# Optimization experiments

Hardware: AMD Instinct MI355X
Metric: run time of the kernel (lower is better)

Reference implementation:

```python
import jax, jax.numpy as jnp
import numpy as np
import itertools


def exclude_mask(n, d):
    # Boolean mask over d object axes of size n: True iff all indices pairwise distinct.
    if d <= 1:
        return jnp.ones((n,) * d, dtype=bool)
    idx = [jnp.arange(n).reshape((1,) * i + (n,) + (1,) * (d - 1 - i)) for i in range(d)]
    m = jnp.ones((n,) * d, dtype=bool)
    for i in range(d):
        for j in range(i + 1, d):
            m = m & (idx[i] != idx[j])
    return m


def reduce_group(x, d, exclude_self=True):
    # x: [B, n^d (d object axes), C] -> [B, n^(d-1), 2C]
    # exists = max over last object axis (masked to 0), forall = min (masked to 1),
    # interleaved per channel as in torch.stack(..., dim=-1).view(..., 2C).
    if exclude_self and d > 1:
        n = x.shape[1]
        m = exclude_mask(n, d)[None, ..., None]
        x0 = jnp.where(m, x, 0.0)
        x1 = jnp.where(m, x, 1.0)
    else:
        x0 = x1 = x
    ex = jnp.max(x0, axis=-2)
    fa = jnp.min(x1, axis=-2)
    out = jnp.stack([ex, fa], axis=-1)  # [..., C, 2]
    return out.reshape(out.shape[:-2] + (out.shape[-2] * 2,))


def expand_group(x, n):
    # Insert a new object axis of size n just before the channel axis (broadcast).
    return jnp.broadcast_to(jnp.expand_dims(x, -2), x.shape[:-1] + (n, x.shape[-1]))


def permute_group(x, d):
    # Concatenate all d! permutations of the last d object axes along channels.
    if d <= 1:
        return x
    nd = x.ndim
    obj_axes = list(range(nd - 1 - d, nd - 1))
    res = []
    for perm in itertools.permutations(obj_axes):
        p = list(range(0, nd - 1 - d)) + list(perm) + [nd - 1]
        res.append(jnp.transpose(x, p))
    return jnp.concatenate(res, axis=-1)


def mlp(x, W1, b1, W2, b2):
    # InferenceLayer: Linear -> ReLU -> Linear -> Sigmoid, applied on channel dim.
    h = jax.nn.relu(x @ W1 + b1)
    return jax.nn.sigmoid(h @ W2 + b2)


def setup_inputs() -> dict:
    key = jax.random.key(0)
    ks = jax.random.split(key, 24)
    B, n, C, H = 4, 48, 16, 64
    cin = {0: 48, 1: 64, 2: 128, 3: 192}
    inp = {
        "x0": jax.random.uniform(ks[0], (B, C), dtype=jnp.float32),
        "x1": jax.random.uniform(ks[1], (B, n, C), dtype=jnp.float32),
        "x2": jax.random.uniform(ks[2], (B, n, n, C), dtype=jnp.float32),
        "x3": jax.random.uniform(ks[3], (B, n, n, n, C), dtype=jnp.float32),
    }
    for g in range(4):
        inp[f"W1_{g}"] = 0.05 * jax.random.normal(ks[4 + 4 * g], (cin[g], H), dtype=jnp.float32)
        inp[f"b1_{g}"] = jnp.zeros((H,), dtype=jnp.float32)
        inp[f"W2_{g}"] = 0.05 * jax.random.normal(ks[5 + 4 * g], (H, C), dtype=jnp.float32)
        inp[f"b2_{g}"] = jnp.zeros((C,), dtype=jnp.float32)
    return inp


def reference(x0, x1, x2, x3,
              W1_0, b1_0, W2_0, b2_0,
              W1_1, b1_1, W2_1, b2_1,
              W1_2, b1_2, W2_2, b2_2,
              W1_3, b1_3, W2_3, b2_3):
    n = x1.shape[1]
    # group 0: [self, reduce(group1)] -> MLP
    t0 = jnp.concatenate([x0, reduce_group(x1, 1)], axis=-1)            # [B, 48]
    o0 = mlp(t0, W1_0, b1_0, W2_0, b2_0)
    # group 1: [expand(group0), self, reduce(group2)] -> MLP (permuter d=1 is identity)
    t1 = jnp.concatenate([expand_group(x0, n), x1, reduce_group(x2, 2)], axis=-1)  # [B,n,64]
    o1 = mlp(t1, W1_1, b1_1, W2_1, b2_1)
    # group 2: [expand(group1), self, reduce(group3)] -> permute(d=2) -> MLP
    t2 = jnp.concatenate([expand_group(x1, n), x2, reduce_group(x3, 3)], axis=-1)  # [B,n,n,64]
    t2 = permute_group(t2, 2)                                           # [B,n,n,128]
    o2 = mlp(t2, W1_2, b1_2, W2_2, b2_2)
    # group 3: [expand(group2), self] -> permute(d=3) -> MLP
    t3 = jnp.concatenate([expand_group(x2, n), x3], axis=-1)            # [B,n,n,n,32]
    t3 = permute_group(t3, 3)                                           # [B,n,n,n,192]
    o3 = mlp(t3, W1_3, b1_3, W2_3, b2_3)
    return (o0, o1, o2, o3)
```

## Files before the change

kernel.cpp:

```cpp
#include <hip/hip_runtime.h>
#include <math.h>

#define NN 48

typedef __attribute__((ext_vector_type(8))) short bf16x8;
typedef __attribute__((ext_vector_type(4))) float f32x4;

__device__ __forceinline__ float sigmoidf_(float x) {
    return 1.0f / (1.0f + __expf(-x));
}

__device__ __forceinline__ unsigned short f2bf(float f) {
    unsigned u = __float_as_uint(f);
    return (unsigned short)((u + 0x7fffu + ((u >> 16) & 1u)) >> 16);
}

__device__ __forceinline__ unsigned packbf2(float a, float b) {
    return (unsigned)f2bf(a) | ((unsigned)f2bf(b) << 16);
}

__global__ __launch_bounds__(256) void k_pre(const float* __restrict__ x3,
                                             const float* __restrict__ W1, const float* __restrict__ W2,
                                             float* __restrict__ r3, unsigned short* __restrict__ wf) {
    int tid = threadIdx.x;
    if (blockIdx.x == 0) {
        for (int e = tid; e < 13312; e += 256) {
            unsigned short v;
            if (e < 12288) {
                int idx = e & 7, l = (e >> 3) & 63, r = e >> 9;
                int ks = r % 6, nt = r / 6;
                v = f2bf(W1[(ks * 32 + ((l >> 4) << 3) + idx) * 64 + (nt << 4) + (l & 15)]);
            } else {
                int e2 = e - 12288;
                int idx = e2 & 7, l = (e2 >> 3) & 63, ks = e2 >> 9;
                v = f2bf(W2[(ks * 32 + ((l >> 4) << 3) + idx) * 16 + (l & 15)]);
            }
            wf[e] = v;
        }
        return;
    }
    int idx = (blockIdx.x - 1) * 256 + tid;
    int cq = idx & 3;
    int pos = idx >> 2;
    int j = pos % NN;
    int i = (pos / NN) % NN;
    const float* base = x3 + (size_t)pos * NN * 16 + (cq << 2);
    float4 ex = make_float4(0.f, 0.f, 0.f, 0.f);
    float4 fa = make_float4(1.f, 1.f, 1.f, 1.f);
    bool dead = (i == j);
    #pragma unroll 8
    for (int k = 0; k < NN; ++k) {
        float4 v = *(const float4*)(base + k * 16);
        bool ok = !dead && (k != i) && (k != j);
        ex.x = fmaxf(ex.x, ok ? v.x : 0.f);  fa.x = fminf(fa.x, ok ? v.x : 1.f);
        ex.y = fmaxf(ex.y, ok ? v.y : 0.f);  fa.y = fminf(fa.y, ok ? v.y : 1.f);
        ex.z = fmaxf(ex.z, ok ? v.z : 0.f);  fa.z = fminf(fa.z, ok ? v.z : 1.f);
        ex.w = fmaxf(ex.w, ok ? v.w : 0.f);  fa.w = fminf(fa.w, ok ? v.w : 1.f);
    }
    float* dst = r3 + (size_t)pos * 32 + (cq << 3);
    *(float4*)dst       = make_float4(ex.x, fa.x, ex.y, fa.y);
    *(float4*)(dst + 4) = make_float4(ex.z, fa.z, ex.w, fa.w);
}

__global__ __launch_bounds__(256) void k_conv(const float* __restrict__ x2, const float* __restrict__ x3,
                                              unsigned short* __restrict__ x2bf,
                                              unsigned short* __restrict__ x3bf) {
    int e = blockIdx.x * 256 + threadIdx.x;
    int stride = gridDim.x * 256;
    for (; e < 1806336; e += stride) {
        const float* src;
        unsigned short* dst;
        if (e < 36864) { int off = e << 2;           src = x2 + off; dst = x2bf + off; }
        else           { int off = (e - 36864) << 2; src = x3 + off; dst = x3bf + off; }
        float4 v = *(const float4*)src;
        uint2 pk;
        pk.x = packbf2(v.x, v.y);
        pk.y = packbf2(v.z, v.w);
        *(uint2*)dst = pk;
    }
}

__global__ __launch_bounds__(256) void k_small(const float* __restrict__ x0, const float* __restrict__ x1,
        const float* __restrict__ x2, const float* __restrict__ r3,
        const float* __restrict__ W1_0, const float* __restrict__ b1_0,
        const float* __restrict__ W2_0, const float* __restrict__ b2_0,
        const float* __restrict__ W1_1, const float* __restrict__ b1_1,
        const float* __restrict__ W2_1, const float* __restrict__ b2_1,
        const float* __restrict__ W1_2, const float* __restrict__ b1_2,
        const float* __restrict__ W2_2, const float* __restrict__ b2_2,
        float* __restrict__ out) {
    __shared__ __align__(16) float smem[8960];
    int tid = threadIdx.x;
    int blk = blockIdx.x;
    if (blk == 0) {
        float* st0 = smem;
        float* sh0 = smem + 192;
        int b = tid >> 6, sub = (tid >> 4) & 3, c = tid & 15;
        float ex = -INFINITY, fa = INFINITY;
        for (int ii = sub * 12; ii < sub * 12 + 12; ++ii) {
            float v = x1[(b * NN + ii) * 16 + c];
            ex = fmaxf(ex, v); fa = fminf(fa, v);
        }
        ex = fmaxf(ex, __shfl_xor(ex, 16)); fa = fminf(fa, __shfl_xor(fa, 16));
        ex = fmaxf(ex, __shfl_xor(ex, 32)); fa = fminf(fa, __shfl_xor(fa, 32));
        if (sub == 0) { st0[b * 48 + 16 + 2 * c] = ex; st0[b * 48 + 17 + 2 * c] = fa; }
        if (tid < 64) st0[(tid >> 4) * 48 + (tid & 15)] = x0[tid];
        __syncthreads();
        {
            int bb = tid >> 6, ln = tid & 63;
            float h = b1_0[ln];
            for (int cc = 0; cc < 48; ++cc) h += st0[bb * 48 + cc] * W1_0[cc * 64 + ln];
            sh0[bb * 64 + ln] = fmaxf(h, 0.f);
        }
        __syncthreads();
        if (tid < 64) {
            int bb = tid >> 4, o = tid & 15;
            float acc = b2_0[o];
            for (int tt = 0; tt < 64; ++tt) acc += sh0[bb * 64 + tt] * W2_0[tt * 16 + o];
            out[bb * 16 + o] = sigmoidf_(acc);
        }
    } else if (blk <= 48) {
        int grp = tid >> 6, ln = tid & 63;
        int row = (blk - 1) * 4 + grp;
        int b = row / NN, i = row % NN;
        float* sin1 = smem + grp * 64;
        float* sh1  = smem + 256 + grp * 64;
        int c = ln & 15, q = ln >> 4;
        float ex = 0.f, fa = 1.f;
        const float* xb = x2 + (size_t)row * NN * 16 + c;
        for (int jj = q * 12; jj < q * 12 + 12; ++jj) {
            float v = xb[jj * 16];
            bool ok = (jj != i);
            ex = fmaxf(ex, ok ? v : 0.f); fa = fminf(fa, ok ? v : 1.f);
        }
        ex = fmaxf(ex, __shfl_xor(ex, 16)); fa = fminf(fa, __shfl_xor(fa, 16));
        ex = fmaxf(ex, __shfl_xor(ex, 32)); fa = fminf(fa, __shfl_xor(fa, 32));
        if (q == 0) { sin1[32 + 2 * c] = ex; sin1[33 + 2 * c] = fa; }
        if (ln < 16) sin1[ln] = x0[b * 16 + ln];
        else if (ln < 32) sin1[ln] = x1[row * 16 + (ln - 16)];
        __syncthreads();
        float h = b1_1[ln];
        #pragma unroll
        for (int c4 = 0; c4 < 64; c4 += 4) {
            float4 iv = *(const float4*)&sin1[c4];
            h += iv.x * W1_1[(c4 + 0) * 64 + ln] + iv.y * W1_1[(c4 + 1) * 64 + ln]
               + iv.z * W1_1[(c4 + 2) * 64 + ln] + iv.w * W1_1[(c4 + 3) * 64 + ln];
        }
        sh1[ln] = fmaxf(h, 0.f);
        __syncthreads();
        if (ln < 16) {
            float acc = b2_1[ln];
            #pragma unroll
            for (int tt = 0; tt < 64; ++tt) acc += sh1[tt] * W2_1[tt * 16 + ln];
            out[64 + row * 16 + ln] = sigmoidf_(acc);
        }
    } else {
        float* sW1  = smem;
        float* sin_ = smem + 8192;
        float* sh   = smem + 8704;
        int wv = tid >> 6, ln = tid & 63;
        for (int p = tid; p < 8192; p += 256) sW1[p] = W1_2[p];
        float bias = b1_2[ln];
        __syncthreads();
        for (int rr = 0; rr < 4; ++rr) {
            int row = (blk - 49) * 16 + rr * 4 + wv;
            int j = row % NN;
            int bi = row / NN;
            int i = bi % NN;
            int b = bi / NN;
            for (int cc = ln; cc < 128; cc += 64) {
                int half = cc >> 6, w = cc & 63;
                int a1 = half ? j : i;
                int a2 = half ? i : j;
                float v;
                if (w < 16)      v = x1[(b * NN + a1) * 16 + w];
                else if (w < 32) v = x2[((b * NN + a1) * NN + a2) * 16 + (w - 16)];
                else             v = r3[((size_t)(b * NN + a1) * NN + a2) * 32 + (w - 32)];
                sin_[wv * 128 + cc] = v;
            }
            __syncthreads();
            float h = bias;
            #pragma unroll
            for (int c4 = 0; c4 < 128; c4 += 4) {
                float4 iv = *(const float4*)&sin_[wv * 128 + c4];
                h += iv.x * sW1[(c4 + 0) * 64 + ln] + iv.y * sW1[(c4 + 1) * 64 + ln]
                   + iv.z * sW1[(c4 + 2) * 64 + ln] + iv.w * sW1[(c4 + 3) * 64 + ln];
            }
            sh[wv * 64 + ln] = fmaxf(h, 0.f);
            __syncthreads();
            if (ln < 16) {
                float acc = b2_2[ln];
                #pragma unroll
                for (int tt = 0; tt < 64; ++tt) acc += sh[wv * 64 + tt] * W2_2[tt * 16 + ln];
                out[3136 + row * 16 + ln] = sigmoidf_(acc);
            }
            __syncthreads();
        }
    }
}

__global__ __launch_bounds__(256) void k_g3d(const unsigned short* __restrict__ x2bf,
        const unsigned short* __restrict__ x3bf, const unsigned short* __restrict__ wf,
        const float* __restrict__ b1, const float* __restrict__ b2,
        float* __restrict__ out3) {
    __shared__ __align__(16) unsigned short sH[2][6 * 64 * 8];

    int tid = threadIdx.x, wv = tid >> 6, l = tid & 63;
    int pp = blockIdx.x, i = 0;
    while (pp >= NN - i) { pp -= NN - i; ++i; }
    int j = i + pp;
    int b = blockIdx.y;

    bf16x8 w1f[6];
    #pragma unroll
    for (int ks = 0; ks < 6; ++ks)
        w1f[ks] = *(const bf16x8*)(wf + (((wv * 6 + ks) << 6) + l) * 8);
    bf16x8 w2f[2];
    #pragma unroll
    for (int ks = 0; ks < 2; ++ks)
        w2f[ks] = *(const bf16x8*)(wf + 12288 + ((ks << 6) + l) * 8);

    const int b2b = b * 36864;
    const int b3b = b * 1769472;
    const int cb2_[6] = { b2b + (i * NN + j) * 16, b2b + i * 768, b2b + (j * NN + i) * 16,
                          b2b + i * 16,            b2b + j * 768, b2b + j * 16 };
    const int cb3_[6] = { b3b + (i * NN + j) * 768, b3b + i * 36864 + j * 16, b3b + (j * NN + i) * 768,
                          b3b + i * 768 + j * 16,   b3b + j * 36864 + i * 16, b3b + j * 768 + i * 16 };
    const int s2_[6] = { 0, 16, 0, 768, 16, 768 };
    const int s3_[6] = { 16, 768, 16, 36864, 768, 36864 };

    int l15 = l & 15, g = l >> 4;
    bool isx2 = (g < 2);
    int goff = (g & 1) << 3;
    const unsigned short* bp = isx2 ? x2bf : x3bf;
    int off_[6], st_[6];
    #pragma unroll
    for (int f = 0; f < 6; ++f) {
        int s = isx2 ? s2_[f] : s3_[f];
        int base = isx2 ? cb2_[f] : cb3_[f];
        off_[f] = base + l15 * s + goff;
        st_[f] = s << 4;
    }

    float bv = b1[(wv << 4) + l15];
    f32x4 acc0_0 = {bv, bv, bv, bv};
    f32x4 acc0_1 = acc0_0, acc0_2 = acc0_0;
    f32x4 acc1_0 = acc0_0, acc1_1 = acc0_0, acc1_2 = acc0_0;
    const int p1[6] = { 2, 4, 0, 5, 1, 3 };

    #pragma unroll
    for (int mt = 0; mt < 3; ++mt) {
        f32x4 a0 = (mt == 0) ? acc0_0 : (mt == 1) ? acc0_1 : acc0_2;
        f32x4 a1 = (mt == 0) ? acc1_0 : (mt == 1) ? acc1_1 : acc1_2;
        #pragma unroll
        for (int f = 0; f < 6; ++f) {
            bf16x8 a = *(const bf16x8*)(bp + off_[f] + mt * st_[f]);
            a0 = __builtin_amdgcn_mfma_f32_16x16x32_bf16(a, w1f[f], a0, 0, 0, 0);
            a1 = __builtin_amdgcn_mfma_f32_16x16x32_bf16(a, w1f[p1[f]], a1, 0, 0, 0);
        }
        if (mt == 0) { acc0_0 = a0; acc1_0 = a1; }
        else if (mt == 1) { acc0_1 = a0; acc1_1 = a1; }
        else { acc0_2 = a0; acc1_2 = a1; }
    }

    {
        int within = ((wv & 1) << 4) + l15;
        int ks2 = wv >> 1;
        int lhi = (within >> 3) << 4;
        int idx = within & 7;
        int rbase = (l >> 4) << 2;
        #pragma unroll
        for (int tr = 0; tr < 2; ++tr) {
            #pragma unroll
            for (int mt = 0; mt < 3; ++mt) {
                f32x4 a = tr ? ((mt == 0) ? acc1_0 : (mt == 1) ? acc1_1 : acc1_2)
                             : ((mt == 0) ? acc0_0 : (mt == 1) ? acc0_1 : acc0_2);
                #pragma unroll
                for (int rg = 0; rg < 4; ++rg) {
                    float h = fmaxf(a[rg], 0.0f);
                    int lp = rbase + rg + lhi;
                    sH[tr][((((mt << 1) + ks2) << 6) + lp) * 8 + idx] = f2bf(h);
                }
            }
        }
    }
    __syncthreads();

    if (wv < 3) {
        float bv2 = b2[l15];
        #pragma unroll
        for (int tr = 0; tr < 2; ++tr) {
            if (tr == 0 || i != j) {
                f32x4 acc = {bv2, bv2, bv2, bv2};
                #pragma unroll
                for (int ks = 0; ks < 2; ++ks) {
                    bf16x8 a = *(const bf16x8*)&sH[tr][((((wv << 1) + ks) << 6) + l) << 3];
                    acc = __builtin_amdgcn_mfma_f32_16x16x32_bf16(a, w2f[ks], acc, 0, 0, 0);
                }
                int triple = tr ? ((b * NN + j) * NN + i) : ((b * NN + i) * NN + j);
                size_t obase = ((size_t)triple * NN + (wv << 4) + ((l >> 4) << 2)) * 16 + l15;
                #pragma unroll
                for (int rg = 0; rg < 4; ++rg)
                    out3[obase + (size_t)rg * 16] = sigmoidf_(acc[rg]);
            }
        }
    }
}

__global__ __launch_bounds__(256) void k_g3m(const float* __restrict__ x2, const float* __restrict__ x3,
                                             const unsigned short* __restrict__ wf,
                                             const float* __restrict__ b1, const float* __restrict__ b2,
                                             float* __restrict__ out3) {
    __shared__ __align__(16) unsigned short sA[18 * 64 * 8];
    __shared__ __align__(16) unsigned short sH[6 * 64 * 8];

    int tid = threadIdx.x;
    int wv = tid >> 6, l = tid & 63;
    int triple = blockIdx.x;
    int j = triple % NN;
    int bi = triple / NN;
    int i = bi % NN;
    int b = bi / NN;

    bf16x8 w1f[6];
    #pragma unroll
    for (int ks = 0; ks < 6; ++ks)
        w1f[ks] = *(const bf16x8*)(wf + (((wv * 6 + ks) << 6) + l) * 8);
    bf16x8 w2f[2];
    #pragma unroll
    for (int ks = 0; ks < 2; ++ks)
        w2f[ks] = *(const bf16x8*)(wf + 12288 + ((ks << 6) + l) * 8);

    const int x2b = b * NN * NN * 16;
    const int x3b = b * NN * NN * NN * 16;

    #pragma unroll
    for (int it = 0; it < 9; ++it) {
        int t = it * 256 + tid;
        int fs = __builtin_amdgcn_readfirstlane(t >> 7);
        int mt = fs / 6;
        int ks = fs - mt * 6;
        int lp = (t >> 1) & 63;
        int kk = (mt << 4) + (lp & 15);
        int w = ((lp >> 4) << 3) + ((t & 1) << 2);
        int a1, a2, a3;
        switch (ks) {
            case 0:  a1 = i;  a2 = j;  a3 = kk; break;
            case 1:  a1 = i;  a2 = kk; a3 = j;  break;
            case 2:  a1 = j;  a2 = i;  a3 = kk; break;
            case 3:  a1 = kk; a2 = i;  a3 = j;  break;
            case 4:  a1 = j;  a2 = kk; a3 = i;  break;
            default: a1 = kk; a2 = j;  a3 = i;  break;
        }
        const float* p2 = x2 + x2b + (a1 * NN + a2) * 16 + w;
        const float* p3 = x3 + x3b + ((a1 * NN + a2) * NN + a3) * 16 + (w - 16);
        const float* p = (w < 16) ? p2 : p3;
        float4 v = *(const float4*)p;
        uint2 pk;
        pk.x = packbf2(v.x, v.y);
        pk.y = packbf2(v.z, v.w);
        *(uint2*)&sA[t * 4] = pk;
    }
    __syncthreads();

    float bv = b1[(wv << 4) + (l & 15)];
    f32x4 acc0 = {bv, bv, bv, bv};
    f32x4 acc1 = acc0, acc2 = acc0;
    #pragma unroll
    for (int ks = 0; ks < 6; ++ks) {
        bf16x8 a0  = *(const bf16x8*)&sA[(((0 * 6 + ks) << 6) + l) << 3];
        bf16x8 a1_ = *(const bf16x8*)&sA[(((1 * 6 + ks) << 6) + l) << 3];
        bf16x8 a2_ = *(const bf16x8*)&sA[(((2 * 6 + ks) << 6) + l) << 3];
        acc0 = __builtin_amdgcn_mfma_f32_16x16x32_bf16(a0,  w1f[ks], acc0, 0, 0, 0);
        acc1 = __builtin_amdgcn_mfma_f32_16x16x32_bf16(a1_, w1f[ks], acc1, 0, 0, 0);
        acc2 = __builtin_amdgcn_mfma_f32_16x16x32_bf16(a2_, w1f[ks], acc2, 0, 0, 0);
    }

    {
        int within = ((wv & 1) << 4) + (l & 15);
        int ks2 = wv >> 1;
        int lhi = (within >> 3) << 4;
        int idx = within & 7;
        int rbase = (l >> 4) << 2;
        #pragma unroll
        for (int mt = 0; mt < 3; ++mt) {
            f32x4 a = (mt == 0) ? acc0 : (mt == 1) ? acc1 : acc2;
            #pragma unroll
            for (int rg = 0; rg < 4; ++rg) {
                float h = fmaxf(a[rg], 0.0f);
                int lp = rbase + rg + lhi;
                sH[((((mt << 1) + ks2) << 6) + lp) * 8 + idx] = f2bf(h);
            }
        }
    }
    __syncthreads();

    if (wv < 3) {
        int mt = wv;
        float bv2 = b2[l & 15];
        f32x4 acc = {bv2, bv2, bv2, bv2};
        #pragma unroll
        for (int ks = 0; ks < 2; ++ks) {
            bf16x8 a = *(const bf16x8*)&sH[((((mt << 1) + ks) << 6) + l) << 3];
            acc = __builtin_amdgcn_mfma_f32_16x16x32_bf16(a, w2f[ks], acc, 0, 0, 0);
        }
        size_t obase = ((size_t)triple * NN + (mt << 4) + ((l >> 4) << 2)) * 16 + (l & 15);
        #pragma unroll
        for (int rg = 0; rg < 4; ++rg)
            out3[obase + (size_t)rg * 16] = sigmoidf_(acc[rg]);
    }
}

extern "C" void kernel_launch(void* const* d_in, const int* in_sizes, int n_in,
                              void* d_out, int out_size, void* d_ws, size_t ws_size,
                              hipStream_t stream) {
    const float* x0 = (const float*)d_in[0];
    const float* x1 = (const float*)d_in[1];
    const float* x2 = (const float*)d_in[2];
    const float* x3 = (const float*)d_in[3];
    const float* W1_0 = (const float*)d_in[4];
    const float* b1_0 = (const float*)d_in[5];
    const float* W2_0 = (const float*)d_in[6];
    const float* b2_0 = (const float*)d_in[7];
    const float* W1_1 = (const float*)d_in[8];
    const float* b1_1 = (const float*)d_in[9];
    const float* W2_1 = (const float*)d_in[10];
    const float* b2_1 = (const float*)d_in[11];
    const float* W1_2 = (const float*)d_in[12];
    const float* b1_2 = (const float*)d_in[13];
    const float* W2_2 = (const float*)d_in[14];
    const float* b2_2 = (const float*)d_in[15];
    const float* W1_3 = (const float*)d_in[16];
    const float* b1_3 = (const float*)d_in[17];
    const float* W2_3 = (const float*)d_in[18];
    const float* b2_3 = (const float*)d_in[19];

    float* out = (float*)d_out;
    float* r3 = (float*)d_ws;
    unsigned short* wf   = (unsigned short*)(r3 + 294912);
    unsigned short* x2bf = wf + 13312;
    unsigned short* x3bf = x2bf + 147456;
    size_t need = (size_t)294912 * 4 + (size_t)(13312 + 147456 + 7077888) * 2;
    int fast = (ws_size >= need) ? 1 : 0;

    hipLaunchKernelGGL(k_pre, dim3(145), dim3(256), 0, stream, x3, W1_3, W2_3, r3, wf);
    if (fast) {
        hipLaunchKernelGGL(k_conv, dim3(1764), dim3(256), 0, stream, x2, x3, x2bf, x3bf);
        hipLaunchKernelGGL(k_g3d, dim3(1176, 4), dim3(256), 0, stream,
                           x2bf, x3bf, wf, b1_3, b2_3, out + 150592);
    } else {
        hipLaunchKernelGGL(k_g3m, dim3(9216), dim3(256), 0, stream,
                           x2, x3, wf, b1_3, b2_3, out + 150592);
    }
    hipLaunchKernelGGL(k_small, dim3(625), dim3(256), 0, stream,
                       x0, x1, x2, r3,
                       W1_0, b1_0, W2_0, b2_0,
                       W1_1, b1_1, W2_1, b2_1,
                       W1_2, b1_2, W2_2, b2_2,
                       out);
}
```

Measured before the change: 90.97 us.

## Fuse bf16 conversion into the x3 reduction pass and rework g3d warp tiling

The x3 reduction kernel now also writes the bf16 copies of x3 and x2, so x3 is read once instead of twice and one launch goes away. The reduction is spread across 64 lanes per position, with shuffle-xor combining replacing the old 48-step serial loop per thread. The main MLP kernel now runs three waves per block, each owning one 16-row M tile and all four N tiles, instead of four waves each owning one N tile over three M tiles. Each wave now keeps all 24 W1 fragments in registers, which increases register pressure.

Measured after the change: 81.00 us. 1.12x faster.

```diff
diff --git a/kernel.cpp b/kernel.cpp
--- a/kernel.cpp
+++ b/kernel.cpp
@@ -19,11 +19,61 @@
     return (unsigned)f2bf(a) | ((unsigned)f2bf(b) << 16);
 }
 
-__global__ __launch_bounds__(256) void k_pre(const float* __restrict__ x3,
-                                             const float* __restrict__ W1, const float* __restrict__ W2,
-                                             float* __restrict__ r3, unsigned short* __restrict__ wf) {
-    int tid = threadIdx.x;
-    if (blockIdx.x == 0) {
+__global__ __launch_bounds__(256) void k_pre(const float* __restrict__ x2, const float* __restrict__ x3,
+        const float* __restrict__ W1, const float* __restrict__ W2,
+        float* __restrict__ r3, unsigned short* __restrict__ wf,
+        unsigned short* __restrict__ x2bf, unsigned short* __restrict__ x3bf, int emit) {
+    int tid = threadIdx.x, blk = blockIdx.x;
+    if (blk < 2304) {
+        int posl = tid >> 6, l = tid & 63;
+        int pos = blk * 4 + posl;
+        int j = pos % NN, i = (pos / NN) % NN;
+        int cq = l & 3, kkb = l >> 2;
+        float4 ex = make_float4(0.f, 0.f, 0.f, 0.f);
+        float4 fa = make_float4(1.f, 1.f, 1.f, 1.f);
+        #pragma unroll
+        for (int s = 0; s < 3; ++s) {
+            int kk = kkb + s * 16;
+            size_t idx = (((size_t)pos * NN + kk) << 4) + (cq << 2);
+            float4 v = *(const float4*)(x3 + idx);
+            if (emit) {
+                uint2 pk;
+                pk.x = packbf2(v.x, v.y);
+                pk.y = packbf2(v.z, v.w);
+                *(uint2*)(x3bf + idx) = pk;
+            }
+            bool ok = (i != j) && (kk != i) && (kk != j);
+            ex.x = fmaxf(ex.x, ok ? v.x : 0.f);  fa.x = fminf(fa.x, ok ? v.x : 1.f);
+            ex.y = fmaxf(ex.y, ok ? v.y : 0.f);  fa.y = fminf(fa.y, ok ? v.y : 1.f);
+            ex.z = fmaxf(ex.z, ok ? v.z : 0.f);  fa.z = fminf(fa.z, ok ? v.z : 1.f);
+            ex.w = fmaxf(ex.w, ok ? v.w : 0.f);  fa.w = fminf(fa.w, ok ? v.w : 1.f);
+        }
+        #pragma unroll
+        for (int m = 4; m <= 32; m <<= 1) {
+            ex.x = fmaxf(ex.x, __shfl_xor(ex.x, m));  fa.x = fminf(fa.x, __shfl_xor(fa.x, m));
+            ex.y = fmaxf(ex.y, __shfl_xor(ex.y, m));  fa.y = fminf(fa.y, __shfl_xor(fa.y, m));
+            ex.z = fmaxf(ex.z, __shfl_xor(ex.z, m));  fa.z = fminf(fa.z, __shfl_xor(fa.z, m));
+            ex.w = fmaxf(ex.w, __shfl_xor(ex.w, m));  fa.w = fminf(fa.w, __shfl_xor(fa.w, m));
+        }
+        if (kkb == 0) {
+            float* dst = r3 + ((size_t)pos << 5) + (cq << 3);
+            *(float4*)dst       = make_float4(ex.x, fa.x, ex.y, fa.y);
+            *(float4*)(dst + 4) = make_float4(ex.z, fa.z, ex.w, fa.w);
+        }
+    } else if (blk < 2340) {
+        if (!emit) return;
+        int bb = blk - 2304;
+        #pragma unroll
+        for (int q = 0; q < 4; ++q) {
+            int e = bb * 1024 + q * 256 + tid;
+            int off = e << 2;
+            float4 v = *(const float4*)(x2 + off);
+            uint2 pk;
+            pk.x = packbf2(v.x, v.y);
+            pk.y = packbf2(v.z, v.w);
+            *(uint2*)(x2bf + off) = pk;
+        }
+    } else {
         for (int e = tid; e < 13312; e += 256) {
             unsigned short v;
             if (e < 12288) {
@@ -37,46 +87,6 @@
             }
             wf[e] = v;
         }
-        return;
-    }
-    int idx = (blockIdx.x - 1) * 256 + tid;
-    int cq = idx & 3;
-    int pos = idx >> 2;
-    int j = pos % NN;
-    int i = (pos / NN) % NN;
-    const float* base = x3 + (size_t)pos * NN * 16 + (cq << 2);
-    float4 ex = make_float4(0.f, 0.f, 0.f, 0.f);
-    float4 fa = make_float4(1.f, 1.f, 1.f, 1.f);
-    bool dead = (i == j);
-    #pragma unroll 8
-    for (int k = 0; k < NN; ++k) {
-        float4 v = *(const float4*)(base + k * 16);
-        bool ok = !dead && (k != i) && (k != j);
-        ex.x = fmaxf(ex.x, ok ? v.x : 0.f);  fa.x = fminf(fa.x, ok ? v.x : 1.f);
-        ex.y = fmaxf(ex.y, ok ? v.y : 0.f);  fa.y = fminf(fa.y, ok ? v.y : 1.f);
-        ex.z = fmaxf(ex.z, ok ? v.z : 0.f);  fa.z = fminf(fa.z, ok ? v.z : 1.f);
-        ex.w = fmaxf(ex.w, ok ? v.w : 0.f);  fa.w = fminf(fa.w, ok ? v.w : 1.f);
-    }
-    float* dst = r3 + (size_t)pos * 32 + (cq << 3);
-    *(float4*)dst       = make_float4(ex.x, fa.x, ex.y, fa.y);
-    *(float4*)(dst + 4) = make_float4(ex.z, fa.z, ex.w, fa.w);
-}
-
-__global__ __launch_bounds__(256) void k_conv(const float* __restrict__ x2, const float* __restrict__ x3,
-                                              unsigned short* __restrict__ x2bf,
-                                              unsigned short* __restrict__ x3bf) {
-    int e = blockIdx.x * 256 + threadIdx.x;
-    int stride = gridDim.x * 256;
-    for (; e < 1806336; e += stride) {
-        const float* src;
-        unsigned short* dst;
-        if (e < 36864) { int off = e << 2;           src = x2 + off; dst = x2bf + off; }
-        else           { int off = (e - 36864) << 2; src = x3 + off; dst = x3bf + off; }
-        float4 v = *(const float4*)src;
-        uint2 pk;
-        pk.x = packbf2(v.x, v.y);
-        pk.y = packbf2(v.z, v.w);
-        *(uint2*)dst = pk;
     }
 }
 
@@ -199,22 +209,24 @@
     }
 }
 
-__global__ __launch_bounds__(256) void k_g3d(const unsigned short* __restrict__ x2bf,
+__global__ __launch_bounds__(192) void k_g3d(const unsigned short* __restrict__ x2bf,
         const unsigned short* __restrict__ x3bf, const unsigned short* __restrict__ wf,
         const float* __restrict__ b1, const float* __restrict__ b2,
         float* __restrict__ out3) {
     __shared__ __align__(16) unsigned short sH[2][6 * 64 * 8];
 
-    int tid = threadIdx.x, wv = tid >> 6, l = tid & 63;
+    int tid = threadIdx.x, mt = tid >> 6, l = tid & 63;
     int pp = blockIdx.x, i = 0;
     while (pp >= NN - i) { pp -= NN - i; ++i; }
     int j = i + pp;
     int b = blockIdx.y;
 
-    bf16x8 w1f[6];
-    #pragma unroll
-    for (int ks = 0; ks < 6; ++ks)
-        w1f[ks] = *(const bf16x8*)(wf + (((wv * 6 + ks) << 6) + l) * 8);
+    bf16x8 w1f[4][6];
+    #pragma unroll
+    for (int nt = 0; nt < 4; ++nt)
+        #pragma unroll
+        for (int ks = 0; ks < 6; ++ks)
+            w1f[nt][ks] = *(const bf16x8*)(wf + (((nt * 6 + ks) << 6) + l) * 8);
     bf16x8 w2f[2];
     #pragma unroll
     for (int ks = 0; ks < 2; ++ks)
@@ -233,51 +245,46 @@
     bool isx2 = (g < 2);
     int goff = (g & 1) << 3;
     const unsigned short* bp = isx2 ? x2bf : x3bf;
-    int off_[6], st_[6];
+    int off_[6];
     #pragma unroll
     for (int f = 0; f < 6; ++f) {
         int s = isx2 ? s2_[f] : s3_[f];
         int base = isx2 ? cb2_[f] : cb3_[f];
-        off_[f] = base + l15 * s + goff;
-        st_[f] = s << 4;
-    }
-
-    float bv = b1[(wv << 4) + l15];
-    f32x4 acc0_0 = {bv, bv, bv, bv};
-    f32x4 acc0_1 = acc0_0, acc0_2 = acc0_0;
-    f32x4 acc1_0 = acc0_0, acc1_1 = acc0_0, acc1_2 = acc0_0;
+        off_[f] = base + ((mt << 4) + l15) * s + goff;
+    }
+
+    f32x4 acc[4][2];
+    #pragma unroll
+    for (int nt = 0; nt < 4; ++nt) {
+        float bv = b1[(nt << 4) + l15];
+        f32x4 t = {bv, bv, bv, bv};
+        acc[nt][0] = t; acc[nt][1] = t;
+    }
     const int p1[6] = { 2, 4, 0, 5, 1, 3 };
 
     #pragma unroll
-    for (int mt = 0; mt < 3; ++mt) {
-        f32x4 a0 = (mt == 0) ? acc0_0 : (mt == 1) ? acc0_1 : acc0_2;
-        f32x4 a1 = (mt == 0) ? acc1_0 : (mt == 1) ? acc1_1 : acc1_2;
-        #pragma unroll
-        for (int f = 0; f < 6; ++f) {
-            bf16x8 a = *(const bf16x8*)(bp + off_[f] + mt * st_[f]);
-            a0 = __builtin_amdgcn_mfma_f32_16x16x32_bf16(a, w1f[f], a0, 0, 0, 0);
-            a1 = __builtin_amdgcn_mfma_f32_16x16x32_bf16(a, w1f[p1[f]], a1, 0, 0, 0);
-        }
-        if (mt == 0) { acc0_0 = a0; acc1_0 = a1; }
-        else if (mt == 1) { acc0_1 = a0; acc1_1 = a1; }
-        else { acc0_2 = a0; acc1_2 = a1; }
+    for (int f = 0; f < 6; ++f) {
+        bf16x8 a = *(const bf16x8*)(bp + off_[f]);
+        #pragma unroll
+        for (int nt = 0; nt < 4; ++nt) {
+            acc[nt][0] = __builtin_amdgcn_mfma_f32_16x16x32_bf16(a, w1f[nt][f], acc[nt][0], 0, 0, 0);
+            acc[nt][1] = __builtin_amdgcn_mfma_f32_16x16x32_bf16(a, w1f[nt][p1[f]], acc[nt][1], 0, 0, 0);
+        }
     }
 
     {
-        int within = ((wv & 1) << 4) + l15;
-        int ks2 = wv >> 1;
-        int lhi = (within >> 3) << 4;
-        int idx = within & 7;
         int rbase = (l >> 4) << 2;
         #pragma unroll
         for (int tr = 0; tr < 2; ++tr) {
             #pragma unroll
-            for (int mt = 0; mt < 3; ++mt) {
-                f32x4 a = tr ? ((mt == 0) ? acc1_0 : (mt == 1) ? acc1_1 : acc1_2)
-                             : ((mt == 0) ? acc0_0 : (mt == 1) ? acc0_1 : acc0_2);
+            for (int nt = 0; nt < 4; ++nt) {
+                int within = ((nt & 1) << 4) + l15;
+                int ks2 = nt >> 1;
+                int lhi = (within >> 3) << 4;
+                int idx = within & 7;
                 #pragma unroll
                 for (int rg = 0; rg < 4; ++rg) {
-                    float h = fmaxf(a[rg], 0.0f);
+                    float h = fmaxf(acc[nt][tr][rg], 0.0f);
                     int lp = rbase + rg + lhi;
                     sH[tr][((((mt << 1) + ks2) << 6) + lp) * 8 + idx] = f2bf(h);
                 }
@@ -286,22 +293,22 @@
     }
     __syncthreads();
 
-    if (wv < 3) {
+    {
         float bv2 = b2[l15];
         #pragma unroll
         for (int tr = 0; tr < 2; ++tr) {
             if (tr == 0 || i != j) {
-                f32x4 acc = {bv2, bv2, bv2, bv2};
+                f32x4 acc2 = {bv2, bv2, bv2, bv2};
                 #pragma unroll
                 for (int ks = 0; ks < 2; ++ks) {
-                    bf16x8 a = *(const bf16x8*)&sH[tr][((((wv << 1) + ks) << 6) + l) << 3];
-                    acc = __builtin_amdgcn_mfma_f32_16x16x32_bf16(a, w2f[ks], acc, 0, 0, 0);
+                    bf16x8 a = *(const bf16x8*)&sH[tr][((((mt << 1) + ks) << 6) + l) << 3];
+                    acc2 = __builtin_amdgcn_mfma_f32_16x16x32_bf16(a, w2f[ks], acc2, 0, 0, 0);
                 }
                 int triple = tr ? ((b * NN + j) * NN + i) : ((b * NN + i) * NN + j);
-                size_t obase = ((size_t)triple * NN + (wv << 4) + ((l >> 4) << 2)) * 16 + l15;
+                size_t obase = ((size_t)triple * NN + (mt << 4) + ((l >> 4) << 2)) * 16 + l15;
                 #pragma unroll
                 for (int rg = 0; rg < 4; ++rg)
-                    out3[obase + (size_t)rg * 16] = sigmoidf_(acc[rg]);
+                    out3[obase + (size_t)rg * 16] = sigmoidf_(acc2[rg]);
             }
         }
     }
@@ -443,15 +450,14 @@
     size_t need = (size_t)294912 * 4 + (size_t)(13312 + 147456 + 7077888) * 2;
     int fast = (ws_size >= need) ? 1 : 0;
 
-    hipLaunchKernelGGL(k_pre, dim3(145), dim3(256), 0, stream, x3, W1_3, W2_3, r3, wf);
-    if (fast) {
-        hipLaunchKernelGGL(k_conv, dim3(1764), dim3(256), 0, stream, x2, x3, x2bf, x3bf);
-        hipLaunchKernelGGL(k_g3d, dim3(1176, 4), dim3(256), 0, stream,
+    hipLaunchKernelGGL(k_pre, dim3(2341), dim3(256), 0, stream,
+                       x2, x3, W1_3, W2_3, r3, wf, x2bf, x3bf, fast);
+    if (fast)
+        hipLaunchKernelGGL(k_g3d, dim3(1176, 4), dim3(192), 0, stream,
                            x2bf, x3bf, wf, b1_3, b2_3, out + 150592);
-    } else {
+    else
         hipLaunchKernelGGL(k_g3m, dim3(9216), dim3(256), 0, stream,
                            x2, x3, wf, b1_3, b2_3, out + 150592);
-    }
     hipLaunchKernelGGL(k_small, dim3(625), dim3(256), 0, stream,
                        x0, x1, x2, r3,
                        W1_0, b1_0, W2_0, b2_0,
```
